# Optimization experiments

Hardware: AMD Instinct MI355X
Metric: run time of the kernel (lower is better)

Reference implementation:

```python
import jax, jax.numpy as jnp
import numpy as np

B, S, E, H, D, W = 2, 4096, 512, 8, 64, 512
NUM_BUCKETS, MAX_DISTANCE = 32, 128  # hardcoded in get_relative_positions for 't5'
NEG_INF = -1e30


def _t5_bucket_causal(relative_position):
    """T5 relative position bucketing, unidirectional (causal)."""
    n = jnp.maximum(-relative_position, 0)
    max_exact = NUM_BUCKETS // 2
    is_small = n < max_exact
    nf = jnp.maximum(n.astype(jnp.float32), 1.0)
    val_if_large = max_exact + (
        jnp.log(nf / max_exact) / np.log(MAX_DISTANCE / max_exact)
        * (NUM_BUCKETS - max_exact)
    ).astype(jnp.int32)
    val_if_large = jnp.minimum(val_if_large, NUM_BUCKETS - 1)
    return jnp.where(is_small, n, val_if_large)


def setup_inputs() -> dict:
    key = jax.random.key(0)
    ks = jax.random.split(key, 7)
    scale = 1.0 / np.sqrt(E)  # keep logits in a sane range
    return {
        'xs': jax.random.normal(ks[0], (B, S, E), jnp.float32),
        'prev_k': jax.random.normal(ks[1], (B, W, H, D), jnp.float32),
        'prev_v': jax.random.normal(ks[2], (B, W, H, D), jnp.float32),
        'w_q': jax.random.normal(ks[3], (E, H, D), jnp.float32) * scale,
        'w_k': jax.random.normal(ks[4], (E, H, D), jnp.float32) * scale,
        'w_v': jax.random.normal(ks[5], (E, H, D), jnp.float32) * scale,
        'rel_bias': jax.random.normal(ks[6], (H, NUM_BUCKETS), jnp.float32),
    }


def reference(xs, prev_k, prev_v, w_q, w_k, w_v, rel_bias):
    nw = S // W  # number of windows
    # kvq projections; queries pre-scaled by 1/sqrt(head_size)
    q = jnp.einsum('bse,ehd->bshd', xs, w_q) * (1.0 / np.sqrt(D))
    k = jnp.einsum('bse,ehd->bshd', xs, w_k)
    v = jnp.einsum('bse,ehd->bshd', xs, w_v)
    qw = q.reshape(B, nw, W, H, D)
    kw = k.reshape(B, nw, W, H, D)
    vw = v.reshape(B, nw, W, H, D)
    # Transformer-XL sliding window: keys for window i = [window i-1 keys ; window i keys]
    k_prev = jnp.concatenate([prev_k[:, None], kw[:, :-1]], axis=1)  # (B,nw,W,H,D)
    v_prev = jnp.concatenate([prev_v[:, None], vw[:, :-1]], axis=1)
    k2 = jnp.concatenate([k_prev, kw], axis=2)  # (B,nw,2W,H,D)
    v2 = jnp.concatenate([v_prev, vw], axis=2)
    # T5 relative position bias and causal mask (num_queries=W, num_keys=2W)
    ctx = jnp.arange(W)[:, None] + W          # query absolute position in key frame
    mem = jnp.arange(2 * W)[None, :]
    relpos = mem - ctx                        # (W, 2W), key - query
    bias = rel_bias[:, _t5_bucket_causal(relpos)]  # (H, W, 2W)
    # causal + window mask: key j attends iff i < j <= i+W (each query sees exactly W keys)
    mask = (relpos <= 0) & (relpos > -W)
    # attention per window
    scores = jnp.einsum('bnqhd,bnkhd->bnhqk', qw, k2)  # (B,nw,H,W,2W)
    scores = scores + bias[None, None]
    scores = jnp.where(mask[None, None, None], scores, NEG_INF)
    probs = jax.nn.softmax(scores, axis=-1)
    attn = jnp.einsum('bnhqk,bnkhd->bnqhd', probs, v2)
    attn_ys = attn.reshape(B, S, H, D)
    # next_kvi cache = last window's keys/values
    next_k = kw[:, -1]
    next_v = vw[:, -1]
    return attn_ys, next_k, next_v
```

## Files before the change

kernel.cpp:

```cpp
#include <hip/hip_runtime.h>
#include <hip/hip_bf16.h>
#include <math.h>

#define B_ 2
#define S_ 4096
#define H_ 8
#define D_ 64
#define W_ 512

#define MASKV -1e30f

typedef float f32x4 __attribute__((ext_vector_type(4)));
typedef short s16x4 __attribute__((ext_vector_type(4)));
typedef short s16x8 __attribute__((ext_vector_type(8)));
typedef unsigned int u32;
typedef __attribute__((address_space(1))) const u32 as1_u32;
typedef __attribute__((address_space(3))) u32 as3_u32;

__device__ inline short f2bf(float f) {
    unsigned u = __builtin_bit_cast(unsigned, f);
    unsigned r = (u + 0x7FFFu + ((u >> 16) & 1u)) >> 16;
    return (short)r;
}
__device__ inline s16x8 pack8(f32x4 a, f32x4 b) {
    s16x8 r;
    r[0]=f2bf(a[0]); r[1]=f2bf(a[1]); r[2]=f2bf(a[2]); r[3]=f2bf(a[3]);
    r[4]=f2bf(b[0]); r[5]=f2bf(b[1]); r[6]=f2bf(b[2]); r[7]=f2bf(b[3]);
    return r;
}
__device__ __forceinline__ void gl_lds16(const void* g, void* l) {
    __builtin_amdgcn_global_load_lds((as1_u32*)(unsigned long long)g,
                                     (as3_u32*)(u32)(unsigned long long)l,
                                     16, 0, 0);
}
__device__ __forceinline__ void drain_vmem() {
    asm volatile("s_waitcnt vmcnt(0)" ::: "memory");
}

__global__ __launch_bounds__(256, 4)
void prep_kernel(const float* __restrict__ xs, const float* __restrict__ pk,
                 const float* __restrict__ pv, const float* __restrict__ wq,
                 const float* __restrict__ wk, const float* __restrict__ wv,
                 short* __restrict__ xsbf, short* __restrict__ pkbf,
                 short* __restrict__ vbt, short* __restrict__ wt)
{
    __shared__ char smem[17408];
    const int bid = blockIdx.x;
    const int tid = threadIdx.x;

    if (bid < 2304) {
        size_t i8 = ((size_t)bid * 256 + tid) * 8;
        const float* src; short* dst; size_t off;
        if (i8 < 4194304) { src = xs; dst = xsbf; off = i8; }
        else              { src = pk; dst = pkbf; off = i8 - 4194304; }
        f32x4 a = *(const f32x4*)(src + off);
        f32x4 b = *(const f32x4*)(src + off + 4);
        *(s16x8*)(dst + off) = pack8(a, b);
    } else if (bid < 2432) {
        short (*st)[72] = (short(*)[72])smem;
        const int b2 = bid - 2304;
        const int jt = b2 & 7, h = (b2 >> 3) & 7, b = b2 >> 6;
        const int jj0 = jt * 64;
        {
            int kk = tid >> 2, d0 = (tid & 3) * 16;
            const float* src = pv + (((size_t)(b * 512 + jj0 + kk)) * 8 + h) * 64 + d0;
            f32x4 x0 = *(const f32x4*)(src);
            f32x4 x1 = *(const f32x4*)(src + 4);
            f32x4 x2 = *(const f32x4*)(src + 8);
            f32x4 x3 = *(const f32x4*)(src + 12);
            *(s16x8*)&st[kk][d0]     = pack8(x0, x1);
            *(s16x8*)&st[kk][d0 + 8] = pack8(x2, x3);
        }
        __syncthreads();
        {
            int dd = tid >> 2, k0 = (tid & 3) * 16;
            s16x8 o0, o1;
            #pragma unroll
            for (int t = 0; t < 8; ++t) { o0[t] = st[k0 + t][dd]; o1[t] = st[k0 + 8 + t][dd]; }
            short* dst = vbt + (size_t)(h * 64 + dd) * 9216 + b * 4608 + jj0 + k0;
            *(s16x8*)dst = o0;
            *(s16x8*)(dst + 8) = o1;
        }
    } else {
        float (*st)[68] = (float(*)[68])smem;
        const int t2 = bid - 2432;
        const int k0 = (t2 & 7) * 64;
        const int nt = t2 >> 3;
        const int z  = nt >> 3;
        const int n0 = (nt & 7) * 64;
        const float* wz = (z == 0) ? wq : (z == 1) ? wk : wv;
        const float scale = (z == 0) ? 0.125f : 1.0f;
        {
            int kk = tid >> 4, nn = (tid & 15) * 4;
            #pragma unroll
            for (int it = 0; it < 4; ++it) {
                f32x4 x = *(const f32x4*)(wz + (size_t)(k0 + kk + it * 16) * 512 + n0 + nn);
                *(f32x4*)&st[kk + it * 16][nn] = x;
            }
        }
        __syncthreads();
        {
            int nn2 = tid >> 2, kseg = (tid & 3) * 16;
            s16x8 o0, o1;
            #pragma unroll
            for (int j = 0; j < 8; ++j) o0[j] = f2bf(st[kseg + j][nn2] * scale);
            #pragma unroll
            for (int j = 0; j < 8; ++j) o1[j] = f2bf(st[kseg + 8 + j][nn2] * scale);
            short* dst = wt + (size_t)(z * 512 + n0 + nn2) * 512 + k0 + kseg;
            *(s16x8*)(dst) = o0;
            *(s16x8*)(dst + 8) = o1;
        }
    }
}

__global__ __launch_bounds__(256, 4)
void proj_kernel(const short* __restrict__ xsbf, const short* __restrict__ wt,
                 short* __restrict__ qkbf, short* __restrict__ vbt,
                 float* __restrict__ out)
{
    __shared__ short Xs[128][64];
    __shared__ short Ws[128][64];

    const int tid = threadIdx.x;
    const int m0  = blockIdx.x * 128;
    const int n0  = blockIdx.y * 128;
    const int z   = n0 >> 9;
    const int ln0 = n0 & 511;
    const int wave = tid >> 6, lane = tid & 63;
    const int wq = (wave & 1) * 64;
    const int wx = (wave >> 1) * 64;
    const int lr = lane & 15, quad = lane >> 4;

    f32x4 acc[4][4] = {};

    const int r8  = lane >> 3;
    const int gr  = lane & 7;

    for (int k0 = 0; k0 < 512; k0 += 64) {
        #pragma unroll
        for (int i = 0; i < 4; ++i) {
            int row = 32 * wave + 8 * i + r8;
            int gs  = gr ^ (row & 7);
            gl_lds16(xsbf + (size_t)(m0 + row) * 512 + k0 + gs * 8, &Xs[32 * wave + 8 * i][0]);
            gl_lds16(wt   + (size_t)(n0 + row) * 512 + k0 + gs * 8, &Ws[32 * wave + 8 * i][0]);
        }
        drain_vmem();
        __syncthreads();
        #pragma unroll
        for (int ks = 0; ks < 2; ++ks) {
            s16x8 af[4], bf[4];
            #pragma unroll
            for (int ta = 0; ta < 4; ++ta) {
                int R = wq + ta * 16 + lr;
                af[ta] = *(const s16x8*)&Ws[R][(((ks * 4 + quad) ^ (R & 7)) * 8)];
            }
            #pragma unroll
            for (int tb = 0; tb < 4; ++tb) {
                int R = wx + tb * 16 + lr;
                bf[tb] = *(const s16x8*)&Xs[R][(((ks * 4 + quad) ^ (R & 7)) * 8)];
            }
            #pragma unroll
            for (int ta = 0; ta < 4; ++ta)
                #pragma unroll
                for (int tb = 0; tb < 4; ++tb)
                    acc[ta][tb] = __builtin_amdgcn_mfma_f32_16x16x32_bf16(
                        af[ta], bf[tb], acc[ta][tb], 0, 0, 0);
        }
        __syncthreads();
    }

    #pragma unroll
    for (int ta = 0; ta < 4; ++ta)
        #pragma unroll
        for (int tb = 0; tb < 4; ++tb) {
            int m  = m0 + wx + tb * 16 + lr;
            int ln = ln0 + wq + ta * 16 + quad * 4;
            int bb = m >> 12, seq = m & 4095;
            if (z < 2) {
                short* base = qkbf + (size_t)z * ((size_t)8192 * 512);
                s16x4 o;
                o[0] = f2bf(acc[ta][tb][0]); o[1] = f2bf(acc[ta][tb][1]);
                o[2] = f2bf(acc[ta][tb][2]); o[3] = f2bf(acc[ta][tb][3]);
                *(s16x4*)(base + (size_t)m * 512 + ln) = o;
                if (z == 1 && seq >= 3584) {
                    float* dst = out + 4194304 + ((size_t)(bb * 512 + seq - 3584)) * 512 + ln;
                    *(f32x4*)dst = acc[ta][tb];
                }
            } else {
                size_t col = (size_t)bb * 4608 + 512 + seq;
                #pragma unroll
                for (int g = 0; g < 4; ++g)
                    vbt[(size_t)(ln + g) * 9216 + col] = f2bf(acc[ta][tb][g]);
                if (seq >= 3584) {
                    float* dst = out + 4194304 + 524288 + ((size_t)(bb * 512 + seq - 3584)) * 512 + ln;
                    *(f32x4*)dst = acc[ta][tb];
                }
            }
        }
}

__global__ __launch_bounds__(512, 4)
void attn_kernel(const short* __restrict__ qkbf, const short* __restrict__ vbt,
                 const short* __restrict__ pkbf, const float* __restrict__ rel_bias,
                 float* __restrict__ out)
{
    __shared__ short k_s[2][64][64];
    __shared__ short vt_s[2][64][64];
    __shared__ short p_s[128][64];
    __shared__ float bias_s[512];

    const short* qb = qkbf;
    const short* kb = qkbf + (size_t)8192 * 512;

    const int bid = blockIdx.x;
    const int qt = bid & 3;
    const int h  = (bid >> 2) & 7;
    const int n  = (bid >> 5) & 7;
    const int b  = bid >> 8;
    const int tid = threadIdx.x;
    const int wave = tid >> 6, lane = tid & 63;
    const int lr = lane & 15, quad = lane >> 4;
    const int q0 = qt * 128;
    const int i0 = q0 + 16 * wave;

    {
        int nd = tid;
        int bucket;
        if (nd < 16) bucket = nd;
        else {
            int vbk = 16 + (int)(log((double)nd * (1.0 / 16.0)) * (16.0 / log(8.0)));
            bucket = vbk < 31 ? vbk : 31;
        }
        bias_s[nd] = rel_bias[h * 32 + bucket];
    }
    const float bias31 = rel_bias[h * 32 + 31];

    s16x8 aq[2];
    {
        const short* src = qb + (size_t)(b * S_ + n * W_ + i0 + lr) * 512 + h * 64 + quad * 8;
        aq[0] = *(const s16x8*)(src);
        aq[1] = *(const s16x8*)(src + 32);
    }

    f32x4 oacc[4] = {};
    float lsum = 0.f;

    const int cmin = (16 * wave) >> 6;
    const int cmax = (16 * wave + 527) >> 6;

    const int r8 = lane >> 3, gr = lane & 7;

    auto issueKV = [&](int c, int pb) {
        int jj = q0 + 64 * c + 8 * wave + r8;
        int p  = n * W_ + jj - W_;
        int gs = gr ^ r8;
        const short* ksrc = (p >= 0)
            ? kb   + ((size_t)(b * S_ + p)) * 512 + h * 64 + gs * 8
            : pkbf + (((size_t)(b * W_ + jj)) * 8 + h) * 64 + gs * 8;
        gl_lds16(ksrc, &k_s[pb][8 * wave][0]);
        int drow = 8 * wave + r8;
        const short* vsrc = vbt + (size_t)(h * 64 + drow) * 9216
                          + b * 4608 + n * W_ + q0 + 64 * c + gs * 8;
        gl_lds16(vsrc, &vt_s[pb][8 * wave][0]);
    };

    issueKV(0, 0);

    for (int c = 0; c < 10; ++c) {
        const int pb = c & 1;
        drain_vmem();
        __syncthreads();
        if (c < 9) issueKV(c + 1, pb ^ 1);
        if (c < cmin || c > cmax) continue;

        f32x4 sacc[4] = {};
        #pragma unroll
        for (int ks = 0; ks < 2; ++ks) {
            s16x8 bk[4];
            #pragma unroll
            for (int tn = 0; tn < 4; ++tn)
                bk[tn] = *(const s16x8*)&k_s[pb][tn * 16 + lr][(((4 * ks + quad) ^ (lr & 7)) * 8)];
            #pragma unroll
            for (int tn = 0; tn < 4; ++tn)
                sacc[tn] = __builtin_amdgcn_mfma_f32_16x16x32_bf16(
                    bk[tn], aq[ks], sacc[tn], 0, 0, 0);
        }

        const int ib = i0 + lr;
        const int jb = q0 + 64 * c;
        if (64 * c - 16 * wave <= 336) {
            #pragma unroll
            for (int tn = 0; tn < 4; ++tn) {
                s16x4 pp;
                #pragma unroll
                for (int rg = 0; rg < 4; ++rg) {
                    int j = jb + tn * 16 + quad * 4 + rg;
                    unsigned dm1 = (unsigned)(j - ib - 1);
                    float sv = (dm1 < 512u) ? (sacc[tn][rg] + bias31) : MASKV;
                    float p = __expf(sv);
                    lsum += p;
                    pp[rg] = f2bf(p);
                }
                int gp = (2 * tn + (quad >> 1)) ^ (lr & 7);
                *(s16x4*)&p_s[16 * wave + lr][gp * 8 + (quad & 1) * 4] = pp;
            }
        } else {
            #pragma unroll
            for (int tn = 0; tn < 4; ++tn) {
                s16x4 pp;
                #pragma unroll
                for (int rg = 0; rg < 4; ++rg) {
                    int j = jb + tn * 16 + quad * 4 + rg;
                    unsigned dm1 = (unsigned)(j - ib - 1);
                    float bias = bias_s[(ib + 512 - j) & 511];
                    float sv = (dm1 < 512u) ? (sacc[tn][rg] + bias) : MASKV;
                    float p = __expf(sv);
                    lsum += p;
                    pp[rg] = f2bf(p);
                }
                int gp = (2 * tn + (quad >> 1)) ^ (lr & 7);
                *(s16x4*)&p_s[16 * wave + lr][gp * 8 + (quad & 1) * 4] = pp;
            }
        }

        asm volatile("s_waitcnt lgkmcnt(0)" ::: "memory");

        #pragma unroll
        for (int ks = 0; ks < 2; ++ks) {
            int gpa = (4 * ks + quad) ^ (lr & 7);
            s16x8 ap = *(const s16x8*)&p_s[16 * wave + lr][gpa * 8];
            s16x8 bv[4];
            #pragma unroll
            for (int tn = 0; tn < 4; ++tn)
                bv[tn] = *(const s16x8*)&vt_s[pb][tn * 16 + lr][(((4 * ks + quad) ^ (lr & 7)) * 8)];
            #pragma unroll
            for (int tn = 0; tn < 4; ++tn)
                oacc[tn] = __builtin_amdgcn_mfma_f32_16x16x32_bf16(
                    ap, bv[tn], oacc[tn], 0, 0, 0);
        }
    }

    lsum += __shfl_xor(lsum, 16);
    lsum += __shfl_xor(lsum, 32);
    float linv[4];
    #pragma unroll
    for (int rg = 0; rg < 4; ++rg)
        linv[rg] = 1.0f / __shfl(lsum, quad * 4 + rg);

    #pragma unroll
    for (int rg = 0; rg < 4; ++rg) {
        int row = i0 + quad * 4 + rg;
        float* dst = out + (((size_t)b * S_ + n * W_ + row) * H_ + h) * D_ + lr;
        #pragma unroll
        for (int tn = 0; tn < 4; ++tn)
            dst[tn * 16] = oacc[tn][rg] * linv[rg];
    }
}

extern "C" void kernel_launch(void* const* d_in, const int* in_sizes, int n_in,
                              void* d_out, int out_size, void* d_ws, size_t ws_size,
                              hipStream_t stream)
{
    const float* xs       = (const float*)d_in[0];
    const float* prev_k   = (const float*)d_in[1];
    const float* prev_v   = (const float*)d_in[2];
    const float* w_q      = (const float*)d_in[3];
    const float* w_k      = (const float*)d_in[4];
    const float* w_v      = (const float*)d_in[5];
    const float* rel_bias = (const float*)d_in[6];
    float* out = (float*)d_out;

    short* xsbf = (short*)d_ws;
    short* wt   = xsbf + (size_t)4194304;
    short* qkbf = wt   + (size_t)786432;
    short* pkbf = qkbf + (size_t)8388608;
    short* vbt  = pkbf + (size_t)524288;

    prep_kernel<<<2624, 256, 0, stream>>>(xs, prev_k, prev_v, w_q, w_k, w_v,
                                          xsbf, pkbf, vbt, wt);

    proj_kernel<<<dim3(64, 12), 256, 0, stream>>>(xsbf, wt, qkbf, vbt, out);

    attn_kernel<<<512, 512, 0, stream>>>(qkbf, vbt, pkbf, rel_bias, out);
}
```

Measured before the change: 128.7 us.

## Double-buffer projection GEMM and use exp2 with packed bf16 conversions

The projection kernel now uses double-buffered LDS tiles with a K step of 32, so the next stage's global-to-LDS load is issued while the current stage's MFMAs run, replacing the load-then-compute loop with two barriers. The attention kernel folds log2(e) into the query weight scale and the bias table, then uses the raw v_exp_f32 (exp2) instruction instead of __expf. Software bf16 rounding is replaced with the hardware v_cvt_pk_bf16_f32 packed conversion in both kernels. The trade-off is smaller K steps with more barriers per tile, and possibly slightly different rounding or denormal behaviour from the hardware instructions.

```diff
diff --git a/kernel.cpp b/kernel.cpp
--- a/kernel.cpp
+++ b/kernel.cpp
@@ -9,11 +9,13 @@
 #define W_ 512
 
 #define MASKV -1e30f
+#define LOG2E 1.4426950408889634f
 
 typedef float f32x4 __attribute__((ext_vector_type(4)));
 typedef short s16x4 __attribute__((ext_vector_type(4)));
 typedef short s16x8 __attribute__((ext_vector_type(8)));
 typedef unsigned int u32;
+typedef unsigned int u32x2 __attribute__((ext_vector_type(2)));
 typedef __attribute__((address_space(1))) const u32 as1_u32;
 typedef __attribute__((address_space(3))) u32 as3_u32;
 
@@ -26,6 +28,16 @@
     s16x8 r;
     r[0]=f2bf(a[0]); r[1]=f2bf(a[1]); r[2]=f2bf(a[2]); r[3]=f2bf(a[3]);
     r[4]=f2bf(b[0]); r[5]=f2bf(b[1]); r[6]=f2bf(b[2]); r[7]=f2bf(b[3]);
+    return r;
+}
+__device__ __forceinline__ u32 cvtpk_bf16(float a, float b) {
+    u32 r;
+    asm("v_cvt_pk_bf16_f32 %0, %1, %2" : "=v"(r) : "v"(a), "v"(b));
+    return r;
+}
+__device__ __forceinline__ float fexp2(float x) {
+    float r;
+    asm("v_exp_f32 %0, %1" : "=v"(r) : "v"(x));
     return r;
 }
 __device__ __forceinline__ void gl_lds16(const void* g, void* l) {
@@ -89,7 +101,7 @@
         const int z  = nt >> 3;
         const int n0 = (nt & 7) * 64;
         const float* wz = (z == 0) ? wq : (z == 1) ? wk : wv;
-        const float scale = (z == 0) ? 0.125f : 1.0f;
+        const float scale = (z == 0) ? 0.125f * LOG2E : 1.0f;
         {
             int kk = tid >> 4, nn = (tid & 15) * 4;
             #pragma unroll
@@ -118,8 +130,8 @@
                  short* __restrict__ qkbf, short* __restrict__ vbt,
                  float* __restrict__ out)
 {
-    __shared__ short Xs[128][64];
-    __shared__ short Ws[128][64];
+    __shared__ short Xs[2][128][32];
+    __shared__ short Ws[2][128][32];
 
     const int tid = threadIdx.x;
     const int m0  = blockIdx.x * 128;
@@ -133,40 +145,46 @@
 
     f32x4 acc[4][4] = {};
 
-    const int r8  = lane >> 3;
-    const int gr  = lane & 7;
-
-    for (int k0 = 0; k0 < 512; k0 += 64) {
-        #pragma unroll
-        for (int i = 0; i < 4; ++i) {
-            int row = 32 * wave + 8 * i + r8;
-            int gs  = gr ^ (row & 7);
-            gl_lds16(xsbf + (size_t)(m0 + row) * 512 + k0 + gs * 8, &Xs[32 * wave + 8 * i][0]);
-            gl_lds16(wt   + (size_t)(n0 + row) * 512 + k0 + gs * 8, &Ws[32 * wave + 8 * i][0]);
-        }
+    const int r4 = lane >> 2;
+    const int g4 = lane & 3;
+
+    auto stage = [&](int s, int buf) {
+        const int k0 = s * 32;
+        #pragma unroll
+        for (int i = 0; i < 2; ++i) {
+            int row = 32 * wave + 16 * i + r4;
+            int gs  = g4 ^ (row & 3);
+            gl_lds16(xsbf + (size_t)(m0 + row) * 512 + k0 + gs * 8,
+                     &Xs[buf][32 * wave + 16 * i][0]);
+            gl_lds16(wt   + (size_t)(n0 + row) * 512 + k0 + gs * 8,
+                     &Ws[buf][32 * wave + 16 * i][0]);
+        }
+    };
+
+    stage(0, 0);
+    for (int s = 0; s < 16; ++s) {
+        const int buf = s & 1;
         drain_vmem();
         __syncthreads();
-        #pragma unroll
-        for (int ks = 0; ks < 2; ++ks) {
-            s16x8 af[4], bf[4];
-            #pragma unroll
-            for (int ta = 0; ta < 4; ++ta) {
-                int R = wq + ta * 16 + lr;
-                af[ta] = *(const s16x8*)&Ws[R][(((ks * 4 + quad) ^ (R & 7)) * 8)];
-            }
-            #pragma unroll
-            for (int tb = 0; tb < 4; ++tb) {
-                int R = wx + tb * 16 + lr;
-                bf[tb] = *(const s16x8*)&Xs[R][(((ks * 4 + quad) ^ (R & 7)) * 8)];
-            }
-            #pragma unroll
-            for (int ta = 0; ta < 4; ++ta)
-                #pragma unroll
-                for (int tb = 0; tb < 4; ++tb)
-                    acc[ta][tb] = __builtin_amdgcn_mfma_f32_16x16x32_bf16(
-                        af[ta], bf[tb], acc[ta][tb], 0, 0, 0);
-        }
-        __syncthreads();
+        if (s < 15) stage(s + 1, buf ^ 1);
+
+        s16x8 af[4], bf[4];
+        #pragma unroll
+        for (int ta = 0; ta < 4; ++ta) {
+            int R = wq + ta * 16 + lr;
+            af[ta] = *(const s16x8*)&Ws[buf][R][((quad ^ (R & 3)) * 8)];
+        }
+        #pragma unroll
+        for (int tb = 0; tb < 4; ++tb) {
+            int R = wx + tb * 16 + lr;
+            bf[tb] = *(const s16x8*)&Xs[buf][R][((quad ^ (R & 3)) * 8)];
+        }
+        #pragma unroll
+        for (int ta = 0; ta < 4; ++ta)
+            #pragma unroll
+            for (int tb = 0; tb < 4; ++tb)
+                acc[ta][tb] = __builtin_amdgcn_mfma_f32_16x16x32_bf16(
+                    af[ta], bf[tb], acc[ta][tb], 0, 0, 0);
     }
 
     #pragma unroll
@@ -178,10 +196,10 @@
             int bb = m >> 12, seq = m & 4095;
             if (z < 2) {
                 short* base = qkbf + (size_t)z * ((size_t)8192 * 512);
-                s16x4 o;
-                o[0] = f2bf(acc[ta][tb][0]); o[1] = f2bf(acc[ta][tb][1]);
-                o[2] = f2bf(acc[ta][tb][2]); o[3] = f2bf(acc[ta][tb][3]);
-                *(s16x4*)(base + (size_t)m * 512 + ln) = o;
+                u32x2 o;
+                o[0] = cvtpk_bf16(acc[ta][tb][0], acc[ta][tb][1]);
+                o[1] = cvtpk_bf16(acc[ta][tb][2], acc[ta][tb][3]);
+                *(u32x2*)(base + (size_t)m * 512 + ln) = o;
                 if (z == 1 && seq >= 3584) {
                     float* dst = out + 4194304 + ((size_t)(bb * 512 + seq - 3584)) * 512 + ln;
                     *(f32x4*)dst = acc[ta][tb];
@@ -231,9 +249,9 @@
             int vbk = 16 + (int)(log((double)nd * (1.0 / 16.0)) * (16.0 / log(8.0)));
             bucket = vbk < 31 ? vbk : 31;
         }
-        bias_s[nd] = rel_bias[h * 32 + bucket];
-    }
-    const float bias31 = rel_bias[h * 32 + 31];
+        bias_s[nd] = rel_bias[h * 32 + bucket] * LOG2E;
+    }
+    const float bias31 = rel_bias[h * 32 + 31] * LOG2E;
 
     s16x8 aq[2];
     {
@@ -291,35 +309,41 @@
         if (64 * c - 16 * wave <= 336) {
             #pragma unroll
             for (int tn = 0; tn < 4; ++tn) {
-                s16x4 pp;
+                float pv[4];
                 #pragma unroll
                 for (int rg = 0; rg < 4; ++rg) {
                     int j = jb + tn * 16 + quad * 4 + rg;
                     unsigned dm1 = (unsigned)(j - ib - 1);
                     float sv = (dm1 < 512u) ? (sacc[tn][rg] + bias31) : MASKV;
-                    float p = __expf(sv);
+                    float p = fexp2(sv);
                     lsum += p;
-                    pp[rg] = f2bf(p);
+                    pv[rg] = p;
                 }
+                u32x2 pp;
+                pp[0] = cvtpk_bf16(pv[0], pv[1]);
+                pp[1] = cvtpk_bf16(pv[2], pv[3]);
                 int gp = (2 * tn + (quad >> 1)) ^ (lr & 7);
-                *(s16x4*)&p_s[16 * wave + lr][gp * 8 + (quad & 1) * 4] = pp;
+                *(u32x2*)&p_s[16 * wave + lr][gp * 8 + (quad & 1) * 4] = pp;
             }
         } else {
             #pragma unroll
             for (int tn = 0; tn < 4; ++tn) {
-                s16x4 pp;
+                float pv[4];
                 #pragma unroll
                 for (int rg = 0; rg < 4; ++rg) {
                     int j = jb + tn * 16 + quad * 4 + rg;
                     unsigned dm1 = (unsigned)(j - ib - 1);
                     float bias = bias_s[(ib + 512 - j) & 511];
                     float sv = (dm1 < 512u) ? (sacc[tn][rg] + bias) : MASKV;
-                    float p = __expf(sv);
+                    float p = fexp2(sv);
                     lsum += p;
-                    pp[rg] = f2bf(p);
+                    pv[rg] = p;
                 }
+                u32x2 pp;
+                pp[0] = cvtpk_bf16(pv[0], pv[1]);
+                pp[1] = cvtpk_bf16(pv[2], pv[3]);
                 int gp = (2 * tn + (quad >> 1)) ^ (lr & 7);
-                *(s16x4*)&p_s[16 * wave + lr][gp * 8 + (quad & 1) * 4] = pp;
+                *(u32x2*)&p_s[16 * wave + lr][gp * 8 + (quad & 1) * 4] = pp;
             }
         }
 
```

After: 131.3 us. 1.02x slower.
